# Optimization experiments

Hardware: AMD Instinct MI355X
Metric: run time of the kernel (lower is better)

Reference implementation:

```python
import jax, jax.numpy as jnp
import numpy as np

D_MODEL = 1024
NUM_HEADS = 16
EPS = 1e-5


def _layernorm(x, gamma, beta):
    mu = jnp.mean(x, axis=-1, keepdims=True)
    var = jnp.mean(jnp.square(x - mu), axis=-1, keepdims=True)
    return (x - mu) * jax.lax.rsqrt(var + EPS) * gamma + beta


def setup_inputs() -> dict:
    key = jax.random.key(0)
    ks = jax.random.split(key, 8)
    B, S, D = 4, 2048, D_MODEL
    xav = (6.0 / (D + D)) ** 0.5  # xavier_uniform bound for square D x D
    inp = {
        "q": jax.random.normal(ks[0], (B, S, D), dtype=jnp.float32),
        "k": jax.random.normal(ks[1], (B, S, D), dtype=jnp.float32),
        "v": jax.random.normal(ks[2], (B, S, D), dtype=jnp.float32),
        "Wq": jax.random.uniform(ks[3], (D, D), jnp.float32, -xav, xav),
        "Wk": jax.random.uniform(ks[4], (D, D), jnp.float32, -xav, xav),
        "Wv": jax.random.uniform(ks[5], (D, D), jnp.float32, -xav, xav),
        "Wo": jax.random.uniform(ks[6], (D, D), jnp.float32, -xav, xav),
        "bo": jnp.zeros((D,), jnp.float32),
        "q_gamma": jnp.ones((D,), jnp.float32),
        "q_beta": jnp.zeros((D,), jnp.float32),
        "k_gamma": jnp.ones((D,), jnp.float32),
        "k_beta": jnp.zeros((D,), jnp.float32),
    }
    return inp


def reference(q, k, v, Wq, Wk, Wv, Wo, bo, q_gamma, q_beta, k_gamma, k_beta):
    B, S, D = q.shape
    H = NUM_HEADS
    scale = 1.0 / (D ** 0.5)  # NOTE: 1/sqrt(d_model), as in the source
    qp = _layernorm(q @ Wq, q_gamma, q_beta)  # LN over full d_model, pre-split
    kp = _layernorm(k @ Wk, k_gamma, k_beta)
    vp = v @ Wv
    qh = qp.reshape(B, S, H, D // H)  # [B,S,H,hd]
    kh = kp.reshape(B, S, H, D // H)
    vh = vp.reshape(B, S, H, D // H)
    attn = jnp.einsum("bqhd,bkhd->bhqk", qh, kh) * scale
    attn = jax.nn.softmax(attn, axis=-1)
    x = jnp.einsum("bhqk,bkhd->bqhd", attn, vh).reshape(B, S, D)
    return x @ Wo + bo
```

## Files before the change

### kernel.cpp

```cpp
#include <hip/hip_runtime.h>
#include <hip/hip_bf16.h>

typedef unsigned short u16;
typedef __attribute__((ext_vector_type(8))) short bf16x8;
typedef __attribute__((ext_vector_type(4))) float f32x4;
typedef __attribute__((ext_vector_type(4))) unsigned short u16x4;
typedef __attribute__((ext_vector_type(4))) unsigned int u32x4;

__device__ __forceinline__ u16 f2b(float f) {
    __hip_bfloat16 h = __float2bfloat16(f);
    u16 r; __builtin_memcpy(&r, &h, 2); return r;
}
__device__ __forceinline__ float bf2f(u16 u) {
    return __uint_as_float(((unsigned)u) << 16);
}
__device__ __forceinline__ void gload16(const void* g, void* l) {
    __builtin_amdgcn_global_load_lds(
        (const __attribute__((address_space(1))) unsigned int*)g,
        (__attribute__((address_space(3))) unsigned int*)l, 16, 0, 0);
}

__global__ __launch_bounds__(256)
void cvt_kernel(const float* __restrict__ in, u16* __restrict__ out) {
    size_t i = ((size_t)blockIdx.x * 256 + threadIdx.x) * 8;
    f32x4 a = *(const f32x4*)(in + i);
    f32x4 b = *(const f32x4*)(in + i + 4);
    u16x4 p0 = { f2b(a[0]), f2b(a[1]), f2b(a[2]), f2b(a[3]) };
    u16x4 p1 = { f2b(b[0]), f2b(b[1]), f2b(b[2]), f2b(b[3]) };
    *(u16x4*)(out + i) = p0;
    *(u16x4*)(out + i + 4) = p1;
}

__global__ __launch_bounds__(256)
void wt_kernel(const float* __restrict__ Wq, const float* __restrict__ Wk,
               const float* __restrict__ Wv, const float* __restrict__ Wo,
               u16* __restrict__ Wt) {
    const float* W = blockIdx.z == 0 ? Wq : blockIdx.z == 1 ? Wk : blockIdx.z == 2 ? Wv : Wo;
    u16* Out = Wt + (size_t)blockIdx.z * (1024 * 1024);
    __shared__ float T[64][65];
    const int t = threadIdx.x;
    const int r0 = blockIdx.y * 64, c0 = blockIdx.x * 64;
#pragma unroll
    for (int e = 0; e < 4; ++e) {
        int row = e * 16 + (t >> 4), c4 = (t & 15) * 4;
        f32x4 v = *(const f32x4*)(W + (r0 + row) * 1024 + c0 + c4);
        T[row][c4] = v[0]; T[row][c4 + 1] = v[1]; T[row][c4 + 2] = v[2]; T[row][c4 + 3] = v[3];
    }
    __syncthreads();
#pragma unroll
    for (int e = 0; e < 4; ++e) {
        int orow = e * 16 + (t >> 4), oc4 = (t & 15) * 4;
        u16x4 pk = { f2b(T[oc4][orow]), f2b(T[oc4 + 1][orow]),
                     f2b(T[oc4 + 2][orow]), f2b(T[oc4 + 3][orow]) };
        *(u16x4*)(Out + (c0 + orow) * 1024 + r0 + oc4) = pk;
    }
}

template <int BIAS>
__global__ __launch_bounds__(256)
void gemm_kernel(const u16* __restrict__ Ab, const u16* __restrict__ Bt,
                 u16* __restrict__ Cb, float* __restrict__ Cf,
                 const float* __restrict__ bias) {
    constexpr int K = 1024;
    __shared__ u16 As[128 * 64];
    __shared__ u16 Bs[128 * 64];
    const int tid = threadIdx.x;
    const int lane = tid & 63, w = tid >> 6;
    const int wr = w >> 1, wc = w & 1;
    const int c = lane & 15, g = lane >> 4;
    const int m0 = blockIdx.y * 128, n0 = blockIdx.x * 128;
    const int sr = lane >> 3, sc = (lane & 7) * 8;
    f32x4 acc[4][4] = {};
    for (int kt = 0; kt < 16; ++kt) {
        const int k0 = kt * 64;
#pragma unroll
        for (int i = 0; i < 4; ++i) {
            int row = 32 * w + 8 * i;
            gload16(Ab + (size_t)(m0 + row + sr) * K + k0 + sc, &As[row * 64]);
            gload16(Bt + (size_t)(n0 + row + sr) * K + k0 + sc, &Bs[row * 64]);
        }
        __syncthreads();
#pragma unroll
        for (int kk = 0; kk < 2; ++kk) {
            bf16x8 af[4], bfr[4];
#pragma unroll
            for (int m = 0; m < 4; ++m)
                af[m] = *(const bf16x8*)&As[(wr * 64 + m * 16 + c) * 64 + kk * 32 + 8 * g];
#pragma unroll
            for (int n = 0; n < 4; ++n)
                bfr[n] = *(const bf16x8*)&Bs[(wc * 64 + n * 16 + c) * 64 + kk * 32 + 8 * g];
#pragma unroll
            for (int m = 0; m < 4; ++m)
#pragma unroll
                for (int n = 0; n < 4; ++n)
                    acc[m][n] = __builtin_amdgcn_mfma_f32_16x16x32_bf16(af[m], bfr[n], acc[m][n], 0, 0, 0);
        }
        __syncthreads();
    }
#pragma unroll
    for (int n = 0; n < 4; ++n) {
        int col = n0 + wc * 64 + n * 16 + c;
        float bv = BIAS ? bias[col] : 0.0f;
#pragma unroll
        for (int m = 0; m < 4; ++m) {
            int row0 = m0 + wr * 64 + m * 16 + 4 * g;
#pragma unroll
            for (int r = 0; r < 4; ++r) {
                if (BIAS) Cf[(row0 + r) * 1024 + col] = acc[m][n][r] + bv;
                else      Cb[(row0 + r) * 1024 + col] = f2b(acc[m][n][r]);
            }
        }
    }
}

__global__ __launch_bounds__(256)
void ln_kernel(const u16* __restrict__ P, const float* __restrict__ gamma,
               const float* __restrict__ beta, float mul, u16* __restrict__ Out) {
    const int row = blockIdx.x;
    const int tid = threadIdx.x;
    const int lane = tid & 63, w = tid >> 6;
    u16x4 xr = *(const u16x4*)(P + row * 1024 + tid * 4);
    float x0 = bf2f(xr[0]), x1 = bf2f(xr[1]), x2 = bf2f(xr[2]), x3 = bf2f(xr[3]);
    float s = x0 + x1 + x2 + x3;
    float sq = x0 * x0 + x1 * x1 + x2 * x2 + x3 * x3;
#pragma unroll
    for (int m = 1; m < 64; m <<= 1) { s += __shfl_xor(s, m); sq += __shfl_xor(sq, m); }
    __shared__ float red[8];
    if (lane == 0) { red[w] = s; red[4 + w] = sq; }
    __syncthreads();
    float st = red[0] + red[1] + red[2] + red[3];
    float sqt = red[4] + red[5] + red[6] + red[7];
    float mu = st * (1.0f / 1024.0f);
    float var = sqt * (1.0f / 1024.0f) - mu * mu;
    float rs = rsqrtf(var + 1e-5f);
    f32x4 gm = *(const f32x4*)(gamma + tid * 4);
    f32x4 bt = *(const f32x4*)(beta + tid * 4);
    float xs[4] = {x0, x1, x2, x3};
    u16x4 pk;
#pragma unroll
    for (int j = 0; j < 4; ++j)
        pk[j] = f2b(((xs[j] - mu) * rs * gm[j] + bt[j]) * mul);
    const int b = row >> 11, sI = row & 2047;
    const int col = tid * 4, hh = col >> 6, d = col & 63;
    *(u16x4*)(Out + (((b * 16 + hh) * 2048 + sI) << 6) + d) = pk;
}

__global__ __launch_bounds__(256)
void vt_kernel(const u16* __restrict__ P, u16* __restrict__ Vt) {
    __shared__ u16 T[64][72];
    const int t = threadIdx.x;
    const int bh = blockIdx.y, s0 = blockIdx.x * 64;
    const int b = bh >> 4, h = bh & 15;
#pragma unroll
    for (int e = 0; e < 4; ++e) {
        int row = e * 16 + (t >> 4), c4 = (t & 15) * 4;
        u16x4 v = *(const u16x4*)(P + (b * 2048 + s0 + row) * 1024 + h * 64 + c4);
        *(u16x4*)&T[row][c4] = v;
    }
    __syncthreads();
#pragma unroll
    for (int e = 0; e < 4; ++e) {
        int dd = e * 16 + (t >> 4), s4 = (t & 15) * 4;
        u16x4 pk = { T[s4][dd], T[s4 + 1][dd], T[s4 + 2][dd], T[s4 + 3][dd] };
        *(u16x4*)(Vt + ((size_t)bh * 64 + dd) * 2048 + s0 + s4) = pk;
    }
}

__global__ __launch_bounds__(256)
void attn_kernel(const u16* __restrict__ Qa, const u16* __restrict__ Ka,
                 const u16* __restrict__ Vt, u16* __restrict__ Xa) {
    __shared__ u16 Ks[2][4096];
    __shared__ u16 Vs[2][4096];
    __shared__ u16 Pl[4][1024];
    const int tid = threadIdx.x;
    const int lane = tid & 63, w = tid >> 6;
    const int c = lane & 15, g = lane >> 4;
    const int bid = blockIdx.x;
    const int bh = (bid & 7) * 8 + ((bid >> 3) & 7);
    const int q0 = (bid >> 6) * 64;
    const int b = bh >> 4, h = bh & 15;

    const int qrow = q0 + w * 16 + c;
    const u16* qptr = Qa + ((size_t)bh * 2048 + qrow) * 64;
    bf16x8 qf0 = *(const bf16x8*)(qptr + 8 * g);
    bf16x8 qf1 = *(const bf16x8*)(qptr + 32 + 8 * g);

    const int sr = lane >> 3;
    const int scg = ((lane & 7) ^ sr) * 8;
    const u16* kA = Ka + ((size_t)bh * 2048 + sr) * 64 + scg;
    const u16* vA = Vt + ((size_t)bh * 64 + sr) * 2048 + scg;
    const int pswz = (c & 7) << 4;

    bf16x8 vones;
#pragma unroll
    for (int j = 0; j < 8; ++j) vones[j] = (short)0x3F80;

    f32x4 o[4] = {};
    f32x4 o4 = {};
    char* pb = (char*)&Pl[w][0];

#pragma unroll
    for (int j = 0; j < 2; ++j) {
        const int m = 2 * w + j;
        gload16(kA + (size_t)(8 * m) * 64, &Ks[0][8 * m * 64]);
        gload16(vA + (size_t)(8 * m) * 2048, &Vs[0][8 * m * 64]);
    }
    __syncthreads();

    int cur = 0;
    for (int t = 0; t < 32; ++t) {
        const int tn = (t + 1) & 31;
#pragma unroll
        for (int j = 0; j < 2; ++j) {
            const int m = 2 * w + j;
            gload16(kA + (size_t)(tn * 64 + 8 * m) * 64, &Ks[cur ^ 1][8 * m * 64]);
            gload16(vA + (size_t)(8 * m) * 2048 + tn * 64, &Vs[cur ^ 1][8 * m * 64]);
        }

        const char* kbase = (const char*)&Ks[cur][0];
        f32x4 sacc[4] = {};
        __builtin_amdgcn_s_setprio(1);
#pragma unroll
        for (int ct = 0; ct < 4; ++ct) {
            const int rb = (c + 16 * ct) * 128;
            bf16x8 kf0 = *(const bf16x8*)(kbase + rb + ((16 * g) ^ pswz));
            bf16x8 kf1 = *(const bf16x8*)(kbase + rb + ((64 + 16 * g) ^ pswz));
            sacc[ct] = __builtin_amdgcn_mfma_f32_16x16x32_bf16(kf0, qf0, sacc[ct], 0, 0, 0);
            sacc[ct] = __builtin_amdgcn_mfma_f32_16x16x32_bf16(kf1, qf1, sacc[ct], 0, 0, 0);
        }
        __builtin_amdgcn_s_setprio(0);

#pragma unroll
        for (int ct = 0; ct < 4; ++ct) {
            float e0 = exp2f(sacc[ct][0]);
            float e1 = exp2f(sacc[ct][1]);
            float e2 = exp2f(sacc[ct][2]);
            float e3 = exp2f(sacc[ct][3]);
            u16x4 pk = { f2b(e0), f2b(e1), f2b(e2), f2b(e3) };
            *(u16x4*)(pb + 128 * c + ((32 * ct + 8 * g) ^ pswz)) = pk;
        }

        const char* vb = (const char*)&Vs[cur][0];
        __builtin_amdgcn_s_setprio(1);
#pragma unroll
        for (int s4 = 0; s4 < 2; ++s4) {
            const int co = ((64 * s4 + 16 * g) ^ pswz);
            bf16x8 af = *(const bf16x8*)(pb + 128 * c + co);
#pragma unroll
            for (int n = 0; n < 4; ++n) {
                bf16x8 vf = *(const bf16x8*)(vb + (c + 16 * n) * 128 + co);
                o[n] = __builtin_amdgcn_mfma_f32_16x16x32_bf16(af, vf, o[n], 0, 0, 0);
            }
            o4 = __builtin_amdgcn_mfma_f32_16x16x32_bf16(af, vones, o4, 0, 0, 0);
        }
        __builtin_amdgcn_s_setprio(0);

        __syncthreads();
        cur ^= 1;
    }

    float iv[4] = { 1.0f / o4[0], 1.0f / o4[1], 1.0f / o4[2], 1.0f / o4[3] };
#pragma unroll
    for (int r = 0; r < 4; ++r) {
        int row = q0 + w * 16 + 4 * g + r;
        u16* xp = Xa + ((size_t)b * 2048 + row) * 1024 + h * 64;
#pragma unroll
        for (int n = 0; n < 4; ++n)
            xp[n * 16 + c] = f2b(o[n][r] * iv[r]);
    }
}

extern "C" void kernel_launch(void* const* d_in, const int* in_sizes, int n_in,
                              void* d_out, int out_size, void* d_ws, size_t ws_size,
                              hipStream_t stream) {
    const float* q   = (const float*)d_in[0];
    const float* k   = (const float*)d_in[1];
    const float* v   = (const float*)d_in[2];
    const float* Wq  = (const float*)d_in[3];
    const float* Wk  = (const float*)d_in[4];
    const float* Wv  = (const float*)d_in[5];
    const float* Wo  = (const float*)d_in[6];
    const float* bo  = (const float*)d_in[7];
    const float* qg  = (const float*)d_in[8];
    const float* qbt = (const float*)d_in[9];
    const float* kg  = (const float*)d_in[10];
    const float* kbt = (const float*)d_in[11];

    char* ws = (char*)d_ws;
    u16* Wt = (u16*)(ws);
    u16* Pb = (u16*)(ws + 8388608);
    u16* Qa = (u16*)(ws + 25165824);
    u16* Ka = (u16*)(ws + 41943040);
    u16* Vt = (u16*)(ws + 58720256);
    u16* Ib = (u16*)(ws + 75497472);
    u16* Xa = Pb;

    const float MUL_Q = 0.04508422002778f;

    wt_kernel<<<dim3(16, 16, 4), 256, 0, stream>>>(Wq, Wk, Wv, Wo, Wt);

    cvt_kernel<<<4096, 256, 0, stream>>>(q, Ib);
    gemm_kernel<0><<<dim3(8, 64), 256, 0, stream>>>(Ib, Wt, Pb, nullptr, nullptr);
    ln_kernel<<<8192, 256, 0, stream>>>(Pb, qg, qbt, MUL_Q, Qa);

    cvt_kernel<<<4096, 256, 0, stream>>>(k, Ib);
    gemm_kernel<0><<<dim3(8, 64), 256, 0, stream>>>(Ib, Wt + 1048576, Pb, nullptr, nullptr);
    ln_kernel<<<8192, 256, 0, stream>>>(Pb, kg, kbt, 1.0f, Ka);

    cvt_kernel<<<4096, 256, 0, stream>>>(v, Ib);
    gemm_kernel<0><<<dim3(8, 64), 256, 0, stream>>>(Ib, Wt + 2097152, Pb, nullptr, nullptr);
    vt_kernel<<<dim3(32, 64), 256, 0, stream>>>(Pb, Vt);

    attn_kernel<<<2048, 256, 0, stream>>>(Qa, Ka, Vt, Xa);

    gemm_kernel<1><<<dim3(8, 64), 256, 0, stream>>>((const u16*)Xa, Wt + 3145728, nullptr, (float*)d_out, bo);
}
```

Baseline: 290.2 us.

## Rework attention kernel to 32x32 MFMA tiles with register-resident P

The attention kernel switches from 16x16x32 to 32x32x16 bf16 MFMA. Each wave now handles 32 query rows, so each block covers 128 queries and the grid is halved. The probability tile stays in registers, repacked with v_cvt_pk_bf16_f32 and permlane32_swap instead of a round trip through LDS. The row-sum moves from an extra MFMA against a ones vector to a VALU accumulation plus a shuffle. This cuts LDS traffic and extra MFMAs and improves K/V reuse per load, but raises register pressure and halves the number of blocks.

```diff
diff --git a/kernel.cpp b/kernel.cpp
--- a/kernel.cpp
+++ b/kernel.cpp
@@ -4,8 +4,10 @@
 typedef unsigned short u16;
 typedef __attribute__((ext_vector_type(8))) short bf16x8;
 typedef __attribute__((ext_vector_type(4))) float f32x4;
+typedef __attribute__((ext_vector_type(16))) float f32x16;
 typedef __attribute__((ext_vector_type(4))) unsigned short u16x4;
 typedef __attribute__((ext_vector_type(4))) unsigned int u32x4;
+typedef __attribute__((ext_vector_type(2))) int i32x2;
 
 __device__ __forceinline__ u16 f2b(float f) {
     __hip_bfloat16 h = __float2bfloat16(f);
@@ -18,6 +20,20 @@
     __builtin_amdgcn_global_load_lds(
         (const __attribute__((address_space(1))) unsigned int*)g,
         (__attribute__((address_space(3))) unsigned int*)l, 16, 0, 0);
+}
+__device__ __forceinline__ unsigned cvtpk(float lo, float hi) {
+    unsigned d;
+    asm("v_cvt_pk_bf16_f32 %0, %1, %2" : "=v"(d) : "v"(lo), "v"(hi));
+    return d;
+}
+__device__ __forceinline__ bf16x8 mk_pa(float a0, float a1, float a2, float a3,
+                                        float b0, float b1, float b2, float b3) {
+    int A0 = (int)cvtpk(a0, a1), A1 = (int)cvtpk(a2, a3);
+    int B0 = (int)cvtpk(b0, b1), B1 = (int)cvtpk(b2, b3);
+    i32x2 r0 = __builtin_amdgcn_permlane32_swap(A0, B0, false, false);
+    i32x2 r1 = __builtin_amdgcn_permlane32_swap(A1, B1, false, false);
+    u32x4 fw = { (unsigned)r0[0], (unsigned)r1[0], (unsigned)r0[1], (unsigned)r1[1] };
+    return __builtin_bit_cast(bf16x8, fw);
 }
 
 __global__ __launch_bounds__(256)
@@ -166,38 +182,34 @@
     }
 }
 
-__global__ __launch_bounds__(256)
+__global__ __launch_bounds__(256, 3)
 void attn_kernel(const u16* __restrict__ Qa, const u16* __restrict__ Ka,
                  const u16* __restrict__ Vt, u16* __restrict__ Xa) {
     __shared__ u16 Ks[2][4096];
     __shared__ u16 Vs[2][4096];
-    __shared__ u16 Pl[4][1024];
     const int tid = threadIdx.x;
     const int lane = tid & 63, w = tid >> 6;
-    const int c = lane & 15, g = lane >> 4;
+    const int col = lane & 31, h = lane >> 5;
     const int bid = blockIdx.x;
     const int bh = (bid & 7) * 8 + ((bid >> 3) & 7);
-    const int q0 = (bid >> 6) * 64;
-    const int b = bh >> 4, h = bh & 15;
-
-    const int qrow = q0 + w * 16 + c;
-    const u16* qptr = Qa + ((size_t)bh * 2048 + qrow) * 64;
-    bf16x8 qf0 = *(const bf16x8*)(qptr + 8 * g);
-    bf16x8 qf1 = *(const bf16x8*)(qptr + 32 + 8 * g);
+    const int q0 = (bid >> 6) * 128;
+    const int b = bh >> 4, hd = bh & 15;
+    const int qb = q0 + w * 32;
+    const int sw = (col & 7) << 4;
+
+    const u16* qptr = Qa + ((size_t)bh * 2048 + qb + col) * 64;
+    bf16x8 qf[4];
+#pragma unroll
+    for (int s = 0; s < 4; ++s)
+        qf[s] = *(const bf16x8*)(qptr + 16 * s + 8 * h);
 
     const int sr = lane >> 3;
     const int scg = ((lane & 7) ^ sr) * 8;
     const u16* kA = Ka + ((size_t)bh * 2048 + sr) * 64 + scg;
     const u16* vA = Vt + ((size_t)bh * 64 + sr) * 2048 + scg;
-    const int pswz = (c & 7) << 4;
-
-    bf16x8 vones;
-#pragma unroll
-    for (int j = 0; j < 8; ++j) vones[j] = (short)0x3F80;
-
-    f32x4 o[4] = {};
-    f32x4 o4 = {};
-    char* pb = (char*)&Pl[w][0];
+
+    f32x16 o0 = {}, o1 = {};
+    float li = 0.f;
 
 #pragma unroll
     for (int j = 0; j < 2; ++j) {
@@ -218,40 +230,40 @@
         }
 
         const char* kbase = (const char*)&Ks[cur][0];
-        f32x4 sacc[4] = {};
+        f32x16 sacc0 = {}, sacc1 = {};
         __builtin_amdgcn_s_setprio(1);
 #pragma unroll
-        for (int ct = 0; ct < 4; ++ct) {
-            const int rb = (c + 16 * ct) * 128;
-            bf16x8 kf0 = *(const bf16x8*)(kbase + rb + ((16 * g) ^ pswz));
-            bf16x8 kf1 = *(const bf16x8*)(kbase + rb + ((64 + 16 * g) ^ pswz));
-            sacc[ct] = __builtin_amdgcn_mfma_f32_16x16x32_bf16(kf0, qf0, sacc[ct], 0, 0, 0);
-            sacc[ct] = __builtin_amdgcn_mfma_f32_16x16x32_bf16(kf1, qf1, sacc[ct], 0, 0, 0);
+        for (int s = 0; s < 4; ++s) {
+            bf16x8 kf0 = *(const bf16x8*)(kbase + (col) * 128       + ((32 * s + 16 * h) ^ sw));
+            bf16x8 kf1 = *(const bf16x8*)(kbase + (32 + col) * 128  + ((32 * s + 16 * h) ^ sw));
+            sacc0 = __builtin_amdgcn_mfma_f32_32x32x16_bf16(kf0, qf[s], sacc0, 0, 0, 0);
+            sacc1 = __builtin_amdgcn_mfma_f32_32x32x16_bf16(kf1, qf[s], sacc1, 0, 0, 0);
         }
         __builtin_amdgcn_s_setprio(0);
 
-#pragma unroll
-        for (int ct = 0; ct < 4; ++ct) {
-            float e0 = exp2f(sacc[ct][0]);
-            float e1 = exp2f(sacc[ct][1]);
-            float e2 = exp2f(sacc[ct][2]);
-            float e3 = exp2f(sacc[ct][3]);
-            u16x4 pk = { f2b(e0), f2b(e1), f2b(e2), f2b(e3) };
-            *(u16x4*)(pb + 128 * c + ((32 * ct + 8 * g) ^ pswz)) = pk;
-        }
+        f32x16 p0, p1;
+#pragma unroll
+        for (int r = 0; r < 16; ++r) { p0[r] = exp2f(sacc0[r]); }
+#pragma unroll
+        for (int r = 0; r < 16; ++r) { p1[r] = exp2f(sacc1[r]); }
+#pragma unroll
+        for (int r = 0; r < 16; ++r) { li += p0[r] + p1[r]; }
+
+        bf16x8 pa0 = mk_pa(p0[0], p0[1], p0[2], p0[3], p0[4], p0[5], p0[6], p0[7]);
+        bf16x8 pa1 = mk_pa(p0[8], p0[9], p0[10], p0[11], p0[12], p0[13], p0[14], p0[15]);
+        bf16x8 pa2 = mk_pa(p1[0], p1[1], p1[2], p1[3], p1[4], p1[5], p1[6], p1[7]);
+        bf16x8 pa3 = mk_pa(p1[8], p1[9], p1[10], p1[11], p1[12], p1[13], p1[14], p1[15]);
 
         const char* vb = (const char*)&Vs[cur][0];
         __builtin_amdgcn_s_setprio(1);
 #pragma unroll
-        for (int s4 = 0; s4 < 2; ++s4) {
-            const int co = ((64 * s4 + 16 * g) ^ pswz);
-            bf16x8 af = *(const bf16x8*)(pb + 128 * c + co);
-#pragma unroll
-            for (int n = 0; n < 4; ++n) {
-                bf16x8 vf = *(const bf16x8*)(vb + (c + 16 * n) * 128 + co);
-                o[n] = __builtin_amdgcn_mfma_f32_16x16x32_bf16(af, vf, o[n], 0, 0, 0);
-            }
-            o4 = __builtin_amdgcn_mfma_f32_16x16x32_bf16(af, vones, o4, 0, 0, 0);
+        for (int sg = 0; sg < 4; ++sg) {
+            bf16x8 pf = sg == 0 ? pa0 : sg == 1 ? pa1 : sg == 2 ? pa2 : pa3;
+            const int cb = (32 * sg + 16 * h) ^ sw;
+            bf16x8 vf0 = *(const bf16x8*)(vb + (col) * 128      + cb);
+            bf16x8 vf1 = *(const bf16x8*)(vb + (32 + col) * 128 + cb);
+            o0 = __builtin_amdgcn_mfma_f32_32x32x16_bf16(pf, vf0, o0, 0, 0, 0);
+            o1 = __builtin_amdgcn_mfma_f32_32x32x16_bf16(pf, vf1, o1, 0, 0, 0);
         }
         __builtin_amdgcn_s_setprio(0);
 
@@ -259,14 +271,16 @@
         cur ^= 1;
     }
 
-    float iv[4] = { 1.0f / o4[0], 1.0f / o4[1], 1.0f / o4[2], 1.0f / o4[3] };
-#pragma unroll
-    for (int r = 0; r < 4; ++r) {
-        int row = q0 + w * 16 + 4 * g + r;
-        u16* xp = Xa + ((size_t)b * 2048 + row) * 1024 + h * 64;
-#pragma unroll
-        for (int n = 0; n < 4; ++n)
-            xp[n * 16 + c] = f2b(o[n][r] * iv[r]);
+    li += __shfl_xor(li, 32);
+    float inv = 1.0f / li;
+#pragma unroll
+    for (int reg = 0; reg < 16; ++reg) {
+        const int crow = (reg & 3) + 8 * (reg >> 2) + 4 * h;
+        float ivr = __shfl(inv, crow);
+        const int row = qb + crow;
+        u16* xp = Xa + ((size_t)b * 2048 + row) * 1024 + hd * 64;
+        xp[col] = f2b(o0[reg] * ivr);
+        xp[32 + col] = f2b(o1[reg] * ivr);
     }
 }
 
@@ -311,7 +325,7 @@
     gemm_kernel<0><<<dim3(8, 64), 256, 0, stream>>>(Ib, Wt + 2097152, Pb, nullptr, nullptr);
     vt_kernel<<<dim3(32, 64), 256, 0, stream>>>(Pb, Vt);
 
-    attn_kernel<<<2048, 256, 0, stream>>>(Qa, Ka, Vt, Xa);
+    attn_kernel<<<1024, 256, 0, stream>>>(Qa, Ka, Vt, Xa);
 
     gemm_kernel<1><<<dim3(8, 64), 256, 0, stream>>>((const u16*)Xa, Wt + 3145728, nullptr, (float*)d_out, bo);
 }
```

Measured after the change: 271.4 us. -6.5%, faster.
